# Kernel tuning notes

Measured on AMD Instinct MI355X. Metric: run time of the kernel, lower is better.

## Reference

```python
import jax, jax.numpy as jnp
import numpy as np

D = 512
B, S1, S2 = 8, 2048, 2048


def setup_inputs() -> dict:
    key = jax.random.key(0)
    ks = jax.random.split(key, 8)
    s = 1.0 / np.sqrt(D)
    return {
        "x1": jax.random.normal(ks[0], (B, S1, D), dtype=jnp.float32),
        "x2": jax.random.normal(ks[1], (B, S2, D), dtype=jnp.float32),
        "Wq": jax.random.normal(ks[2], (D, D), dtype=jnp.float32) * s,
        "bq": jnp.zeros((D,), dtype=jnp.float32),
        "Wk": jax.random.normal(ks[3], (D, D), dtype=jnp.float32) * s,
        "bk": jnp.zeros((D,), dtype=jnp.float32),
        "Wv": jax.random.normal(ks[4], (D, D), dtype=jnp.float32) * s,
        "bv": jnp.zeros((D,), dtype=jnp.float32),
    }


def reference(x1, x2, Wq, bq, Wk, bk, Wv, bv):
    # q,k,v projections (torch Linear: x @ W^T + b)
    q = jnp.einsum("bsd,ed->bse", x1, Wq) + bq  # [B,S1,D]
    k = jnp.einsum("btd,ed->bte", x2, Wk) + bk  # [B,S2,D]
    v = jnp.einsum("btd,ed->bte", x2, Wv) + bv  # [B,S2,D]
    # NOTE: source scales by input_dim (D), not sqrt(D)
    scores = jnp.einsum("bse,bte->bst", q, k) / D  # [B,S1,S2]
    attn = jax.nn.softmax(scores, axis=-1)
    return jnp.einsum("bst,bte->bse", attn, v)  # [B,S1,D]
```

## Files before the change

### kernel.cpp

```cpp
#include <hip/hip_runtime.h>

using u8  = unsigned char;
using u16 = unsigned short;
using u32 = unsigned int;
using s16x8 = __attribute__((ext_vector_type(8))) short;
using bf16x8 = __attribute__((ext_vector_type(8))) __bf16;
using f32x4 = __attribute__((ext_vector_type(4))) float;
using i32x4 = __attribute__((ext_vector_type(4))) int;
using i32x8 = __attribute__((ext_vector_type(8))) int;

__device__ inline u16 f2bf(float f) {
  u32 u = __float_as_uint(f);
  u = (u + 0x7FFFu + ((u >> 16) & 1u)) >> 16;
  return (u16)u;
}

__device__ inline u8 f2fp8(float f) {
  return (u8)(__builtin_amdgcn_cvt_pk_fp8_f32(f, f, 0, false) & 0xFF);
}

__device__ inline f32x4 mfma16(s16x8 a, s16x8 b, f32x4 c) {
  return __builtin_amdgcn_mfma_f32_16x16x32_bf16(
      __builtin_bit_cast(bf16x8, a), __builtin_bit_cast(bf16x8, b), c, 0, 0, 0);
}

__device__ inline f32x4 mfma_fp8(i32x8 a, i32x8 b, f32x4 c) {
  return __builtin_amdgcn_mfma_scale_f32_16x16x128_f8f6f4(
      a, b, c, 0 , 0 , 0, 127, 0, 127);
}

__device__ inline void load_lds16(const void* g, void* l) {
  __builtin_amdgcn_global_load_lds(
      (const __attribute__((address_space(1))) void*)g,
      (__attribute__((address_space(3))) void*)l, 16, 0, 0);
}

__global__ __launch_bounds__(256) void cast_x12(
    const float* __restrict__ x1, const float* __restrict__ x2,
    u16* __restrict__ o1, u16* __restrict__ o2) {
  const float* in = blockIdx.y ? x2 : x1;
  u16* out = blockIdx.y ? o2 : o1;
  int i = (blockIdx.x * 256 + threadIdx.x) * 4;
  float4 f = *(const float4*)(in + i);
  ushort4 o;
  o.x = f2bf(f.x); o.y = f2bf(f.y); o.z = f2bf(f.z); o.w = f2bf(f.w);
  *(ushort4*)(out + i) = o;
}

__global__ __launch_bounds__(256) void cast_w3z(
    const float* __restrict__ a, const float* __restrict__ b,
    const float* __restrict__ c, u16* __restrict__ oa, u16* __restrict__ ob,
    u16* __restrict__ oc, float* __restrict__ lbuf) {
  if (blockIdx.y == 3) {
    if (blockIdx.x < 64) lbuf[blockIdx.x * 256 + threadIdx.x] = 0.0f;
    return;
  }
  const float* in = blockIdx.y == 0 ? a : (blockIdx.y == 1 ? b : c);
  u16* out = blockIdx.y == 0 ? oa : (blockIdx.y == 1 ? ob : oc);
  int i = (blockIdx.x * 256 + threadIdx.x) * 4;
  float4 f = *(const float4*)(in + i);
  ushort4 o;
  o.x = f2bf(f.x); o.y = f2bf(f.y); o.z = f2bf(f.z); o.w = f2bf(f.w);
  *(ushort4*)(out + i) = o;
}

template <int EPI>
__global__ __launch_bounds__(256) void gemm64(
    const u16* __restrict__ A, const u16* __restrict__ B,
    const u16* __restrict__ B2, void* __restrict__ C, void* __restrict__ C2,
    const float* __restrict__ bias, const float* __restrict__ bias2,
    const float* __restrict__ lsum,
    int M, int N, int K, long sA, long sB, long sC) {
  const int bz = blockIdx.z;
  const int m0 = blockIdx.y * 128;
  const int n0 = blockIdx.x * 128;
  const u16* Ab = A + (size_t)bz * sA;
  const u16* Bsel = (EPI == 4 && n0 >= 512) ? B2 : B;
  const int nb = (EPI == 4 && n0 >= 512) ? n0 - 512 : n0;
  const u16* Bb = Bsel + (size_t)bz * sB;
  const int tid = threadIdx.x;
  const int lane = tid & 63;
  const int wave = tid >> 6;
  const int wm = (wave >> 1) * 64;
  const int wn = (wave & 1) * 64;

  __shared__ u16 SM[128 * 64 * 2];
  u16* As = SM;
  u16* Bs = SM + 128 * 64;

  const int sr = lane >> 3;
  const int gd = (lane & 7) ^ sr;
  const int ch0 = wave * 4;

  f32x4 acc[4][4];
#pragma unroll
  for (int i = 0; i < 4; ++i)
#pragma unroll
    for (int j = 0; j < 4; ++j) acc[i][j] = 0.0f;

  const int fr = lane & 15;
  const int fg = lane >> 4;

  for (int k0 = 0; k0 < K; k0 += 64) {
#pragma unroll
    for (int it = 0; it < 4; ++it) {
      const int ch = ch0 + it;
      const int row = ch * 8 + sr;
      load_lds16(Ab + (size_t)(m0 + row) * K + k0 + gd * 8, &As[ch * 512]);
      load_lds16(Bb + (size_t)(nb + row) * K + k0 + gd * 8, &Bs[ch * 512]);
    }
    __syncthreads();
#pragma unroll
    for (int s = 0; s < 2; ++s) {
      const int slot = ((s * 4 + fg) ^ (fr & 7)) * 8;
      s16x8 af[4], bfr[4];
#pragma unroll
      for (int i = 0; i < 4; ++i) {
        af[i]  = *(const s16x8*)&As[(wm + i * 16 + fr) * 64 + slot];
        bfr[i] = *(const s16x8*)&Bs[(wn + i * 16 + fr) * 64 + slot];
      }
#pragma unroll
      for (int mi = 0; mi < 4; ++mi)
#pragma unroll
        for (int ni = 0; ni < 4; ++ni)
          acc[mi][ni] = mfma16(af[mi], bfr[ni], acc[mi][ni]);
    }
    __syncthreads();
  }

  const int er = fg * 4;
  const int ec = fr;

  if (EPI == 0) {
    u8* Cb = (u8*)C;
#pragma unroll
    for (int mi = 0; mi < 4; ++mi)
#pragma unroll
      for (int ni = 0; ni < 4; ++ni) {
        const int col = n0 + wn + ni * 16 + ec;
        const float badd = bias[col];
#pragma unroll
        for (int i = 0; i < 4; ++i) {
          const int row = m0 + wm + mi * 16 + er + i;
          Cb[(size_t)row * N + col] = f2fp8(acc[mi][ni][i] + badd);
        }
      }
  } else if (EPI == 4) {
    if (n0 < 512) {
      u8* Cb = (u8*)C;
#pragma unroll
      for (int mi = 0; mi < 4; ++mi)
#pragma unroll
        for (int ni = 0; ni < 4; ++ni) {
          const int col = n0 + wn + ni * 16 + ec;
          const float badd = bias[col];
#pragma unroll
          for (int i = 0; i < 4; ++i) {
            const int row = m0 + wm + mi * 16 + er + i;
            Cb[(size_t)row * 512 + col] = f2fp8(acc[mi][ni][i] + badd);
          }
        }
    } else {
      u16* Tb = SM;
      const int batch = m0 >> 11;
      const int srow = m0 & 2047;
      u16* Cv = (u16*)C2 + (size_t)batch * (512 * 2048);
#pragma unroll
      for (int h = 0; h < 2; ++h) {
        if ((wn >> 6) == h) {
#pragma unroll
          for (int mi = 0; mi < 4; ++mi)
#pragma unroll
            for (int ni = 0; ni < 4; ++ni) {
              const int c = ni * 16 + ec;
              const float badd = bias2[n0 - 512 + wn + c];
#pragma unroll
              for (int i = 0; i < 4; ++i) {
                const int r = wm + mi * 16 + er + i;
                Tb[c * 136 + r] = f2bf(acc[mi][ni][i] + badd);
              }
            }
        }
        __syncthreads();
        const int d = tid >> 2;
        const int sc = (tid & 3) * 32;
        const int dglob = n0 - 512 + 64 * h + d;
#pragma unroll
        for (int j = 0; j < 4; ++j) {
          uint4 v = *(const uint4*)&Tb[d * 136 + sc + j * 8];
          *(uint4*)&Cv[(size_t)dglob * 2048 + srow + sc + j * 8] = v;
        }
        __syncthreads();
      }
    }
  } else {
    float* Cb = (float*)C + (size_t)bz * sC;
#pragma unroll
    for (int mi = 0; mi < 4; ++mi)
#pragma unroll
      for (int i = 0; i < 4; ++i) {
        const int row = m0 + wm + mi * 16 + er + i;
        const float li = __builtin_amdgcn_rcpf(lsum[(size_t)bz * M + row]);
#pragma unroll
        for (int ni = 0; ni < 4; ++ni) {
          const int col = n0 + wn + ni * 16 + ec;
          Cb[(size_t)row * N + col] = acc[mi][ni][i] * li;
        }
      }
  }
}

__global__ __launch_bounds__(256) void gemm_fp8_scores(
    const u8* __restrict__ A, const u8* __restrict__ B, u16* __restrict__ C,
    float* __restrict__ lsum, float scale,
    int M, int N, int K, long sA, long sB, long sC) {
  const int bz = blockIdx.z;
  const int m0 = blockIdx.y * 128;
  const int n0 = blockIdx.x * 128;
  const u8* Ab = A + (size_t)bz * sA;
  const u8* Bb = B + (size_t)bz * sB;
  const int tid = threadIdx.x;
  const int lane = tid & 63;
  const int wave = tid >> 6;
  const int wm = (wave >> 1) * 64;
  const int wn = (wave & 1) * 64;

  __shared__ u8 As8[128 * 128];
  __shared__ u8 Bs8[128 * 128];

  const int sr = lane >> 3;
  const int gd = (lane & 7) ^ sr;
  const int ch0 = wave * 4;

  f32x4 acc[4][4];
#pragma unroll
  for (int i = 0; i < 4; ++i)
#pragma unroll
    for (int j = 0; j < 4; ++j) acc[i][j] = 0.0f;

  const int fr = lane & 15;
  const int fg = lane >> 4;
  const int r7 = fr & 7;
  const int s0 = (2 * fg) ^ r7;
  const int s1 = s0 ^ 1;

  for (int k0 = 0; k0 < K; k0 += 128) {
#pragma unroll
    for (int it = 0; it < 4; ++it) {
      const int ch = ch0 + it;
      const int row = ch * 8 + sr;
      load_lds16(Ab + (size_t)(m0 + row) * K + k0 + gd * 16, &As8[ch * 1024]);
      load_lds16(Bb + (size_t)(n0 + row) * K + k0 + gd * 16, &Bs8[ch * 1024]);
    }
    __syncthreads();
    i32x8 af[4], bfv[4];
#pragma unroll
    for (int i = 0; i < 4; ++i) {
      const u8* pa = &As8[(wm + i * 16 + fr) * 128];
      i32x4 alo = *(const i32x4*)(pa + s0 * 16);
      i32x4 ahi = *(const i32x4*)(pa + s1 * 16);
      af[i][0] = alo[0]; af[i][1] = alo[1]; af[i][2] = alo[2]; af[i][3] = alo[3];
      af[i][4] = ahi[0]; af[i][5] = ahi[1]; af[i][6] = ahi[2]; af[i][7] = ahi[3];
      const u8* pb = &Bs8[(wn + i * 16 + fr) * 128];
      i32x4 blo = *(const i32x4*)(pb + s0 * 16);
      i32x4 bhi = *(const i32x4*)(pb + s1 * 16);
      bfv[i][0] = blo[0]; bfv[i][1] = blo[1]; bfv[i][2] = blo[2]; bfv[i][3] = blo[3];
      bfv[i][4] = bhi[0]; bfv[i][5] = bhi[1]; bfv[i][6] = bhi[2]; bfv[i][7] = bhi[3];
    }
#pragma unroll
    for (int mi = 0; mi < 4; ++mi)
#pragma unroll
      for (int ni = 0; ni < 4; ++ni)
        acc[mi][ni] = mfma_fp8(af[mi], bfv[ni], acc[mi][ni]);
    __syncthreads();
  }

  const int er = fg * 4;
  const int ec = fr;
  u16* Cb = C + (size_t)bz * sC;
#pragma unroll
  for (int mi = 0; mi < 4; ++mi) {
    float rs[4] = {0.0f, 0.0f, 0.0f, 0.0f};
#pragma unroll
    for (int ni = 0; ni < 4; ++ni) {
      const int col = n0 + wn + ni * 16 + ec;
#pragma unroll
      for (int i = 0; i < 4; ++i) {
        const float p = __expf(acc[mi][ni][i] * scale);
        rs[i] += p;
        Cb[(size_t)(m0 + wm + mi * 16 + er + i) * N + col] = f2bf(p);
      }
    }
#pragma unroll
    for (int i = 0; i < 4; ++i) {
      rs[i] += __shfl_xor(rs[i], 1);
      rs[i] += __shfl_xor(rs[i], 2);
      rs[i] += __shfl_xor(rs[i], 4);
      rs[i] += __shfl_xor(rs[i], 8);
    }
    if (ec == 0) {
#pragma unroll
      for (int i = 0; i < 4; ++i)
        atomicAdd(&lsum[(size_t)bz * M + m0 + wm + mi * 16 + er + i], rs[i]);
    }
  }
}

extern "C" void kernel_launch(void* const* d_in, const int* in_sizes, int n_in,
                              void* d_out, int out_size, void* d_ws, size_t ws_size,
                              hipStream_t stream) {
  constexpr int B = 8, S = 2048, D = 512;
  constexpr size_t MS = (size_t)B * S;

  const float* x1 = (const float*)d_in[0];
  const float* x2 = (const float*)d_in[1];
  const float* Wq = (const float*)d_in[2];
  const float* bq = (const float*)d_in[3];
  const float* Wk = (const float*)d_in[4];
  const float* bk = (const float*)d_in[5];
  const float* Wv = (const float*)d_in[6];
  const float* bv = (const float*)d_in[7];
  float* out = (float*)d_out;

  u16* x1b = (u16*)d_ws;
  u16* x2b = x1b + MS * D;
  u16* Wqb = x2b + MS * D;
  u16* Wkb = Wqb + (size_t)D * D;
  u16* Wvb = Wkb + (size_t)D * D;
  u16* vTb = Wvb + (size_t)D * D;
  u16* Sc  = vTb + MS * D;
  float* lbuf = (float*)(Sc + (size_t)B * S * S);
  u8* qb8 = (u8*)(lbuf + MS);
  u8* kb8 = qb8 + MS * D;

  dim3 blk(256);

  cast_x12<<<dim3((MS * D) / 1024, 2), blk, 0, stream>>>(x1, x2, x1b, x2b);
  cast_w3z<<<dim3((D * D) / 1024, 4), blk, 0, stream>>>(
      Wq, Wk, Wv, Wqb, Wkb, Wvb, lbuf);

  gemm64<0><<<dim3(4, 128, 1), blk, 0, stream>>>(
      x1b, Wqb, nullptr, qb8, nullptr, bq, nullptr, nullptr,
      16384, 512, 512, 0, 0, 0);

  gemm64<4><<<dim3(8, 128, 1), blk, 0, stream>>>(
      x2b, Wkb, Wvb, kb8, vTb, bk, bv, nullptr,
      16384, 512, 512, 0, 0, 0);

  gemm_fp8_scores<<<dim3(16, 16, B), blk, 0, stream>>>(
      qb8, kb8, Sc, lbuf, 1.0f / (float)D, 2048, 2048, 512,
      (long)S * D, (long)S * D, (long)S * S);

  gemm64<3><<<dim3(4, 16, B), blk, 0, stream>>>(
      Sc, vTb, nullptr, out, nullptr, nullptr, nullptr, lbuf,
      2048, 512, 2048, (long)S * S, (long)D * S, (long)S * D);
}
```

Measured before the change: 267.9 us.

## Fuse scores, softmax and PV into one flash-style attention kernel

```diff
diff --git a/kernel.cpp b/kernel.cpp
--- a/kernel.cpp
+++ b/kernel.cpp
@@ -50,11 +50,7 @@
 __global__ __launch_bounds__(256) void cast_w3z(
     const float* __restrict__ a, const float* __restrict__ b,
     const float* __restrict__ c, u16* __restrict__ oa, u16* __restrict__ ob,
-    u16* __restrict__ oc, float* __restrict__ lbuf) {
-  if (blockIdx.y == 3) {
-    if (blockIdx.x < 64) lbuf[blockIdx.x * 256 + threadIdx.x] = 0.0f;
-    return;
-  }
+    u16* __restrict__ oc) {
   const float* in = blockIdx.y == 0 ? a : (blockIdx.y == 1 ? b : c);
   u16* out = blockIdx.y == 0 ? oa : (blockIdx.y == 1 ? ob : oc);
   int i = (blockIdx.x * 256 + threadIdx.x) * 4;
@@ -69,11 +65,13 @@
     const u16* __restrict__ A, const u16* __restrict__ B,
     const u16* __restrict__ B2, void* __restrict__ C, void* __restrict__ C2,
     const float* __restrict__ bias, const float* __restrict__ bias2,
-    const float* __restrict__ lsum,
     int M, int N, int K, long sA, long sB, long sC) {
   const int bz = blockIdx.z;
-  const int m0 = blockIdx.y * 128;
-  const int n0 = blockIdx.x * 128;
+  const int nwg = gridDim.x * gridDim.y;
+  int flat = blockIdx.x + gridDim.x * blockIdx.y;
+  flat = (flat & 7) * (nwg >> 3) + (flat >> 3);
+  const int m0 = (flat / gridDim.x) * 128;
+  const int n0 = (flat % gridDim.x) * 128;
   const u16* Ab = A + (size_t)bz * sA;
   const u16* Bsel = (EPI == 4 && n0 >= 512) ? B2 : B;
   const int nb = (EPI == 4 && n0 >= 512) ? n0 - 512 : n0;
@@ -145,7 +143,7 @@
           Cb[(size_t)row * N + col] = f2fp8(acc[mi][ni][i] + badd);
         }
       }
-  } else if (EPI == 4) {
+  } else {
     if (n0 < 512) {
       u8* Cb = (u8*)C;
 #pragma unroll
@@ -193,117 +191,167 @@
         __syncthreads();
       }
     }
-  } else {
-    float* Cb = (float*)C + (size_t)bz * sC;
-#pragma unroll
-    for (int mi = 0; mi < 4; ++mi)
-#pragma unroll
-      for (int i = 0; i < 4; ++i) {
-        const int row = m0 + wm + mi * 16 + er + i;
-        const float li = __builtin_amdgcn_rcpf(lsum[(size_t)bz * M + row]);
-#pragma unroll
-        for (int ni = 0; ni < 4; ++ni) {
-          const int col = n0 + wn + ni * 16 + ec;
-          Cb[(size_t)row * N + col] = acc[mi][ni][i] * li;
-        }
-      }
   }
 }
 
-__global__ __launch_bounds__(256) void gemm_fp8_scores(
-    const u8* __restrict__ A, const u8* __restrict__ B, u16* __restrict__ C,
-    float* __restrict__ lsum, float scale,
-    int M, int N, int K, long sA, long sB, long sC) {
-  const int bz = blockIdx.z;
-  const int m0 = blockIdx.y * 128;
-  const int n0 = blockIdx.x * 128;
-  const u8* Ab = A + (size_t)bz * sA;
-  const u8* Bb = B + (size_t)bz * sB;
+__global__ __launch_bounds__(512, 2) void attn_fused(
+    const u8* __restrict__ q8, const u8* __restrict__ k8,
+    const u16* __restrict__ vT, float* __restrict__ out) {
+  const int batch = blockIdx.x;
+  const int q0 = blockIdx.y * 64;
+  const u8* qb = q8 + ((size_t)batch * 2048 + q0) * 512;
+  const u8* kb = k8 + (size_t)batch * 2048 * 512;
+  const u16* vb = vT + (size_t)batch * 512 * 2048;
+  float* ob = out + ((size_t)batch * 2048 + q0) * 512;
+
   const int tid = threadIdx.x;
   const int lane = tid & 63;
   const int wave = tid >> 6;
-  const int wm = (wave >> 1) * 64;
-  const int wn = (wave & 1) * 64;
-
-  __shared__ u8 As8[128 * 128];
-  __shared__ u8 Bs8[128 * 128];
-
+  const int wm = (wave >> 2) * 32;
+  const int wn = (wave & 3) * 32;
   const int sr = lane >> 3;
   const int gd = (lane & 7) ^ sr;
-  const int ch0 = wave * 4;
-
-  f32x4 acc[4][4];
-#pragma unroll
-  for (int i = 0; i < 4; ++i)
-#pragma unroll
-    for (int j = 0; j < 4; ++j) acc[i][j] = 0.0f;
-
   const int fr = lane & 15;
   const int fg = lane >> 4;
   const int r7 = fr & 7;
   const int s0 = (2 * fg) ^ r7;
   const int s1 = s0 ^ 1;
 
-  for (int k0 = 0; k0 < K; k0 += 128) {
-#pragma unroll
-    for (int it = 0; it < 4; ++it) {
-      const int ch = ch0 + it;
-      const int row = ch * 8 + sr;
-      load_lds16(Ab + (size_t)(m0 + row) * K + k0 + gd * 16, &As8[ch * 1024]);
-      load_lds16(Bb + (size_t)(n0 + row) * K + k0 + gd * 16, &Bs8[ch * 1024]);
-    }
+  __shared__ u8 Ks[4][16384];
+  __shared__ u16 Ps[64 * 128];
+  __shared__ float l_lds[64];
+  if (tid < 64) l_lds[tid] = 0.0f;
+
+  i32x8 Qf[2][4];
+#pragma unroll
+  for (int mi = 0; mi < 2; ++mi)
+#pragma unroll
+    for (int kc = 0; kc < 4; ++kc) {
+      const u8* p = qb + (size_t)(wm + mi * 16 + fr) * 512 + kc * 128 + fg * 32;
+      i32x4 lo = *(const i32x4*)p;
+      i32x4 hi = *(const i32x4*)(p + 16);
+      i32x8 q;
+      q[0] = lo[0]; q[1] = lo[1]; q[2] = lo[2]; q[3] = lo[3];
+      q[4] = hi[0]; q[5] = hi[1]; q[6] = hi[2]; q[7] = hi[3];
+      Qf[mi][kc] = q;
+    }
+
+#pragma unroll
+  for (int it = 0; it < 8; ++it) {
+    const int idx = wave * 8 + it;
+    const int kc = idx >> 4, sub = idx & 15;
+    load_lds16(kb + (size_t)(sub * 8 + sr) * 512 + kc * 128 + gd * 16,
+               &Ks[kc][sub * 1024]);
+  }
+  __syncthreads();
+
+  f32x4 oacc[4][4];
+#pragma unroll
+  for (int i = 0; i < 4; ++i)
+#pragma unroll
+    for (int j = 0; j < 4; ++j) oacc[i][j] = 0.0f;
+  float l_reg[2][4] = {{0.0f, 0.0f, 0.0f, 0.0f}, {0.0f, 0.0f, 0.0f, 0.0f}};
+
+  for (int t = 0; t < 16; ++t) {
+    const int kv0 = t * 128;
+
+    f32x4 sacc[2][2];
+#pragma unroll
+    for (int i = 0; i < 2; ++i)
+#pragma unroll
+      for (int j = 0; j < 2; ++j) sacc[i][j] = 0.0f;
+#pragma unroll
+    for (int kc = 0; kc < 4; ++kc) {
+      i32x8 bf2[2];
+#pragma unroll
+      for (int ni = 0; ni < 2; ++ni) {
+        const u8* pb = &Ks[kc][(wn + ni * 16 + fr) * 128];
+        i32x4 blo = *(const i32x4*)(pb + s0 * 16);
+        i32x4 bhi = *(const i32x4*)(pb + s1 * 16);
+        i32x8 b;
+        b[0] = blo[0]; b[1] = blo[1]; b[2] = blo[2]; b[3] = blo[3];
+        b[4] = bhi[0]; b[5] = bhi[1]; b[6] = bhi[2]; b[7] = bhi[3];
+        bf2[ni] = b;
+      }
+#pragma unroll
+      for (int mi = 0; mi < 2; ++mi)
+#pragma unroll
+        for (int ni = 0; ni < 2; ++ni)
+          sacc[mi][ni] = mfma_fp8(Qf[mi][kc], bf2[ni], sacc[mi][ni]);
+    }
+
+#pragma unroll
+    for (int mi = 0; mi < 2; ++mi)
+#pragma unroll
+      for (int ni = 0; ni < 2; ++ni) {
+        const int c = wn + ni * 16 + fr;
+        const int g = c >> 3;
+        const int co = c & 7;
+#pragma unroll
+        for (int i = 0; i < 4; ++i) {
+          const int r = wm + mi * 16 + fg * 4 + i;
+          const float p = __expf(sacc[mi][ni][i] * (1.0f / 512.0f));
+          Ps[r * 128 + ((g ^ (r & 7)) << 3) + co] = f2bf(p);
+          l_reg[mi][i] += p;
+        }
+      }
     __syncthreads();
-    i32x8 af[4], bfv[4];
-#pragma unroll
-    for (int i = 0; i < 4; ++i) {
-      const u8* pa = &As8[(wm + i * 16 + fr) * 128];
-      i32x4 alo = *(const i32x4*)(pa + s0 * 16);
-      i32x4 ahi = *(const i32x4*)(pa + s1 * 16);
-      af[i][0] = alo[0]; af[i][1] = alo[1]; af[i][2] = alo[2]; af[i][3] = alo[3];
-      af[i][4] = ahi[0]; af[i][5] = ahi[1]; af[i][6] = ahi[2]; af[i][7] = ahi[3];
-      const u8* pb = &Bs8[(wn + i * 16 + fr) * 128];
-      i32x4 blo = *(const i32x4*)(pb + s0 * 16);
-      i32x4 bhi = *(const i32x4*)(pb + s1 * 16);
-      bfv[i][0] = blo[0]; bfv[i][1] = blo[1]; bfv[i][2] = blo[2]; bfv[i][3] = blo[3];
-      bfv[i][4] = bhi[0]; bfv[i][5] = bhi[1]; bfv[i][6] = bhi[2]; bfv[i][7] = bhi[3];
-    }
-#pragma unroll
-    for (int mi = 0; mi < 4; ++mi)
-#pragma unroll
-      for (int ni = 0; ni < 4; ++ni)
-        acc[mi][ni] = mfma_fp8(af[mi], bfv[ni], acc[mi][ni]);
+
+    if (t < 15) {
+#pragma unroll
+      for (int it = 0; it < 8; ++it) {
+        const int idx = wave * 8 + it;
+        const int kc = idx >> 4, sub = idx & 15;
+        load_lds16(
+            kb + (size_t)(kv0 + 128 + sub * 8 + sr) * 512 + kc * 128 + gd * 16,
+            &Ks[kc][sub * 1024]);
+      }
+    }
+
+#pragma unroll
+    for (int ks = 0; ks < 4; ++ks) {
+      s16x8 pa[4];
+#pragma unroll
+      for (int mi = 0; mi < 4; ++mi) {
+        const int r = mi * 16 + fr;
+        pa[mi] = *(const s16x8*)&Ps[r * 128 + (((ks * 4 + fg) ^ (r & 7)) << 3)];
+      }
+#pragma unroll
+      for (int ni = 0; ni < 4; ++ni) {
+        const int d = wave * 64 + ni * 16 + fr;
+        const s16x8 bv =
+            *(const s16x8*)&vb[(size_t)d * 2048 + kv0 + ks * 32 + fg * 8];
+#pragma unroll
+        for (int mi = 0; mi < 4; ++mi)
+          oacc[mi][ni] = mfma16(pa[mi], bv, oacc[mi][ni]);
+      }
+    }
     __syncthreads();
   }
 
-  const int er = fg * 4;
-  const int ec = fr;
-  u16* Cb = C + (size_t)bz * sC;
-#pragma unroll
-  for (int mi = 0; mi < 4; ++mi) {
-    float rs[4] = {0.0f, 0.0f, 0.0f, 0.0f};
-#pragma unroll
-    for (int ni = 0; ni < 4; ++ni) {
-      const int col = n0 + wn + ni * 16 + ec;
-#pragma unroll
-      for (int i = 0; i < 4; ++i) {
-        const float p = __expf(acc[mi][ni][i] * scale);
-        rs[i] += p;
-        Cb[(size_t)(m0 + wm + mi * 16 + er + i) * N + col] = f2bf(p);
-      }
-    }
+#pragma unroll
+  for (int mi = 0; mi < 2; ++mi)
 #pragma unroll
     for (int i = 0; i < 4; ++i) {
-      rs[i] += __shfl_xor(rs[i], 1);
-      rs[i] += __shfl_xor(rs[i], 2);
-      rs[i] += __shfl_xor(rs[i], 4);
-      rs[i] += __shfl_xor(rs[i], 8);
-    }
-    if (ec == 0) {
-#pragma unroll
-      for (int i = 0; i < 4; ++i)
-        atomicAdd(&lsum[(size_t)bz * M + m0 + wm + mi * 16 + er + i], rs[i]);
-    }
-  }
+      float rs = l_reg[mi][i];
+      rs += __shfl_xor(rs, 1);
+      rs += __shfl_xor(rs, 2);
+      rs += __shfl_xor(rs, 4);
+      rs += __shfl_xor(rs, 8);
+      if (fr == 0) atomicAdd(&l_lds[wm + mi * 16 + fg * 4 + i], rs);
+    }
+  __syncthreads();
+
+#pragma unroll
+  for (int mi = 0; mi < 4; ++mi)
+#pragma unroll
+    for (int i = 0; i < 4; ++i) {
+      const int r = mi * 16 + fg * 4 + i;
+      const float li = __builtin_amdgcn_rcpf(l_lds[r]);
+#pragma unroll
+      for (int ni = 0; ni < 4; ++ni)
+        ob[(size_t)r * 512 + wave * 64 + ni * 16 + fr] = oacc[mi][ni][i] * li;
+    }
 }
 
 extern "C" void kernel_launch(void* const* d_in, const int* in_sizes, int n_in,
@@ -336,22 +384,16 @@
   dim3 blk(256);
 
   cast_x12<<<dim3((MS * D) / 1024, 2), blk, 0, stream>>>(x1, x2, x1b, x2b);
-  cast_w3z<<<dim3((D * D) / 1024, 4), blk, 0, stream>>>(
-      Wq, Wk, Wv, Wqb, Wkb, Wvb, lbuf);
+  cast_w3z<<<dim3((D * D) / 1024, 3), blk, 0, stream>>>(
+      Wq, Wk, Wv, Wqb, Wkb, Wvb);
 
   gemm64<0><<<dim3(4, 128, 1), blk, 0, stream>>>(
-      x1b, Wqb, nullptr, qb8, nullptr, bq, nullptr, nullptr,
+      x1b, Wqb, nullptr, qb8, nullptr, bq, nullptr,
       16384, 512, 512, 0, 0, 0);
 
   gemm64<4><<<dim3(8, 128, 1), blk, 0, stream>>>(
-      x2b, Wkb, Wvb, kb8, vTb, bk, bv, nullptr,
+      x2b, Wkb, Wvb, kb8, vTb, bk, bv,
       16384, 512, 512, 0, 0, 0);
 
-  gemm_fp8_scores<<<dim3(16, 16, B), blk, 0, stream>>>(
-      qb8, kb8, Sc, lbuf, 1.0f / (float)D, 2048, 2048, 512,
-      (long)S * D, (long)S * D, (long)S * S);
-
-  gemm64<3><<<dim3(4, 16, B), blk, 0, stream>>>(
-      Sc, vTb, nullptr, out, nullptr, nullptr, nullptr, lbuf,
-      2048, 512, 2048, (long)S * S, (long)D * S, (long)S * D);
-}
+  attn_fused<<<dim3(8, 32, 1), dim3(512), 0, stream>>>(qb8, kb8, vTb, out);
+}
```

After: 272.3 us. No clear change (+1.6%).
